# Kernel optimization log

Measured on AMD Instinct MI355X. Metric: run time of the kernel, lower is better.

The kernel has to match this reference:

```python
import jax, jax.numpy as jnp
import numpy as np

B, T, D = 8, 2048, 1024   # batch, seq_len (== block_size), n_embed
HS = 128                   # head_size

def setup_inputs() -> dict:
    key = jax.random.key(0)
    kx, kk, kq, kv = jax.random.split(key, 4)
    s = D ** -0.5  # torch Linear default init scale ~ U(-1/sqrt(in), 1/sqrt(in))
    x  = jax.random.normal(kx, (B, T, D), dtype=jnp.float32)
    Wk = jax.random.uniform(kk, (HS, D), jnp.float32, -s, s)
    Wq = jax.random.uniform(kq, (HS, D), jnp.float32, -s, s)
    Wv = jax.random.uniform(kv, (HS, D), jnp.float32, -s, s)
    return {"x": x, "Wk": Wk, "Wq": Wq, "Wv": Wv}

def reference(x, Wk, Wq, Wv):
    # single-head causal self-attention; dropout disabled (eval mode)
    Tlen = x.shape[1]
    k = jnp.einsum('btd,hd->bth', x, Wk)   # [B,T,HS]
    q = jnp.einsum('btd,hd->bth', x, Wq)
    v = jnp.einsum('btd,hd->bth', x, Wv)
    scale = Wk.shape[0] ** -0.5
    scores = jnp.einsum('bth,bsh->bts', q, k) * scale   # [B,T,T]
    causal = jnp.tril(jnp.ones((Tlen, Tlen), dtype=bool))
    scores = jnp.where(causal, scores, -jnp.inf)
    weights = jax.nn.softmax(scores, axis=-1)
    out = jnp.einsum('bts,bsh->bth', weights, v)        # [B,T,HS]
    return out
```

## Files before the change

kernel.cpp:

```cpp
#include <hip/hip_runtime.h>
#include <hip/hip_bf16.h>
#include <math.h>

#define BATCH_N 8
#define SEQ_T   2048
#define DIM_D   1024
#define HS_N    128

using bf16x8_t = __attribute__((ext_vector_type(8))) __bf16;
using bf16x4_t = __attribute__((ext_vector_type(4))) __bf16;
using f32x4_t  = __attribute__((ext_vector_type(4))) float;

__device__ __forceinline__ f32x4_t mfma_16x16x32(bf16x8_t a, bf16x8_t b, f32x4_t c) {
  return __builtin_amdgcn_mfma_f32_16x16x32_bf16(a, b, c, 0, 0, 0);
}

__device__ __forceinline__ void async_cp16(const void* g, void* l) {
  __builtin_amdgcn_global_load_lds(
      (const __attribute__((address_space(1))) unsigned int*)g,
      (__attribute__((address_space(3))) unsigned int*)l, 16, 0, 0);
}

#define BAR()      __builtin_amdgcn_s_barrier()
#define FENCE()    asm volatile("" ::: "memory")
#define WAIT_VM(n) asm volatile("s_waitcnt vmcnt(" #n ")" ::: "memory")
#define WAIT_LGKM0 asm volatile("s_waitcnt lgkmcnt(0)" ::: "memory")

__global__ __launch_bounds__(256) void castw_kernel(
    const float* __restrict__ Wk, const float* __restrict__ Wq,
    const float* __restrict__ Wv, __bf16* __restrict__ Wb,
    unsigned int* __restrict__ km) {
  if (blockIdx.x == 0 && threadIdx.x < 8) km[threadIdx.x] = 0u;
  int idx = blockIdx.x * 256 + threadIdx.x;
  int e   = idx * 4;
  int row = e >> 10;
  int col = e & 1023;
  const float* src;
  float sc = 1.0f;
  if (row < 128) {
    src = Wk + row * DIM_D + col;
  } else if (row < 256) {
    src = Wq + (row - 128) * DIM_D + col;
    sc  = 0.08838834764831845f;
  } else {
    src = Wv + (row - 256) * DIM_D + col;
  }
  float4 v = *(const float4*)src;
  bf16x4_t o;
  o[0] = (__bf16)(v.x * sc); o[1] = (__bf16)(v.y * sc);
  o[2] = (__bf16)(v.z * sc); o[3] = (__bf16)(v.w * sc);
  *(bf16x4_t*)(Wb + e) = o;
}

__global__ __launch_bounds__(512, 1) void proj_kernel(
    const float* __restrict__ x, const __bf16* __restrict__ Wb,
    __bf16* __restrict__ Qb, __bf16* __restrict__ Kb, __bf16* __restrict__ Vt,
    unsigned int* __restrict__ km) {
  __shared__ __align__(16) char psmem[139264];
  __bf16* A = (__bf16*)psmem;

  const int tid  = threadIdx.x;
  const int lane = tid & 63;
  const int wave = tid >> 6;
  const int h    = wave >> 2;
  const int g    = wave & 3;
  const int lr = lane & 15;
  const int lq = lane >> 4;
  const int m0 = blockIdx.x * 64;

  f32x4_t acc[2][6];
  #pragma unroll
  for (int mt = 0; mt < 2; ++mt)
    #pragma unroll
    for (int nt = 0; nt < 6; ++nt) acc[mt][nt] = (f32x4_t){0.f, 0.f, 0.f, 0.f};

  auto stageB = [&](int kt) {
    __bf16* Bs = (__bf16*)(psmem + 65536 + (kt % 3) * 24576);
    for (int c = wave; c < 24; c += 8) {
      const int row = c * 16 + (lane >> 2);
      const int u   = (lane & 3) ^ ((row >> 1) & 3);
      async_cp16(Wb + (size_t)row * DIM_D + kt * 32 + u * 8, Bs + c * 512);
    }
  };

  stageB(0);
  stageB(1);

  for (int p = 0; p < 2; ++p) {
    __syncthreads();

    {
      const int r  = tid >> 3;
      const int t  = tid & 7;
      const float* xs = x + (size_t)(m0 + r) * DIM_D + p * 512;
      __bf16* as = A + r * 512;
      const int sw = r & 7;
      #pragma unroll
      for (int i = 0; i < 8; ++i) {
        const int u = t + 8 * i;
        float4 f0 = *(const float4*)(xs + u * 8);
        float4 f1 = *(const float4*)(xs + u * 8 + 4);
        bf16x8_t a;
        a[0] = (__bf16)f0.x; a[1] = (__bf16)f0.y;
        a[2] = (__bf16)f0.z; a[3] = (__bf16)f0.w;
        a[4] = (__bf16)f1.x; a[5] = (__bf16)f1.y;
        a[6] = (__bf16)f1.z; a[7] = (__bf16)f1.w;
        *(bf16x8_t*)(as + ((u ^ sw) * 8)) = a;
      }
    }
    __syncthreads();

    for (int kt2 = 0; kt2 < 16; ++kt2) {
      const int kt = p * 16 + kt2;
      if (kt + 2 < 32) stageB(kt + 2);
      if (kt < 30)       { WAIT_VM(6); }
      else if (kt == 30) { WAIT_VM(3); }
      else               { WAIT_VM(0); }
      BAR();
      FENCE();
      const __bf16* Bs = (const __bf16*)(psmem + 65536 + (kt % 3) * 24576);

      bf16x8_t af[2];
      #pragma unroll
      for (int mt = 0; mt < 2; ++mt) {
        const int ml = h * 32 + mt * 16 + lr;
        const int u  = kt2 * 4 + lq;
        af[mt] = *(const bf16x8_t*)(&A[ml * 512 + ((u ^ (ml & 7)) * 8)]);
      }
      bf16x8_t bfv[6];
      #pragma unroll
      for (int nt = 0; nt < 6; ++nt) {
        const int nl = g * 96 + nt * 16 + lr;
        bfv[nt] = *(const bf16x8_t*)(&Bs[nl * 32 + ((lq ^ ((nl >> 1) & 3)) * 8)]);
      }
      #pragma unroll
      for (int mt = 0; mt < 2; ++mt)
        #pragma unroll
        for (int nt = 0; nt < 6; ++nt)
          acc[mt][nt] = mfma_16x16x32(af[mt], bfv[nt], acc[mt][nt]);
      WAIT_LGKM0;
      BAR();
      FENCE();
    }
  }

  __syncthreads();
  float* rowss = (float*)psmem;
  if (tid < 64) rowss[tid] = 0.f;
  __syncthreads();
  if (g < 2) {
    #pragma unroll
    for (int mt = 0; mt < 2; ++mt)
      #pragma unroll
      for (int r = 0; r < 4; ++r) {
        float s = 0.f;
        #pragma unroll
        for (int nt = 0; nt < 6; ++nt)
          if (g == 0 || nt < 2) s += acc[mt][nt][r] * acc[mt][nt][r];
        s += __shfl_xor(s, 1); s += __shfl_xor(s, 2);
        s += __shfl_xor(s, 4); s += __shfl_xor(s, 8);
        if (lr == 0) atomicAdd(&rowss[h * 32 + mt * 16 + lq * 4 + r], s);
      }
  }
  __syncthreads();
  if (tid < 64) {
    float v = rowss[tid];
    #pragma unroll
    for (int off = 1; off < 64; off <<= 1) v = fmaxf(v, __shfl_xor(v, off));
    if (tid == 0) atomicMax(km + (m0 >> 11), __float_as_uint(v));
  }

  #pragma unroll
  for (int mt = 0; mt < 2; ++mt) {
    const int t0 = m0 + h * 32 + mt * 16 + lq * 4;
    #pragma unroll
    for (int nt = 0; nt < 6; ++nt) {
      const int nn = g * 96 + nt * 16 + lr;
      if (nn < 256) {
        __bf16* dst = (nn < 128) ? (Kb + nn) : (Qb + (nn - 128));
        #pragma unroll
        for (int r = 0; r < 4; ++r)
          dst[(size_t)(t0 + r) * HS_N] = (__bf16)acc[mt][nt][r];
      } else {
        const int bb = t0 >> 11;
        const int tl = t0 & 2047;
        bf16x4_t o;
        #pragma unroll
        for (int r = 0; r < 4; ++r) o[r] = (__bf16)acc[mt][nt][r];
        *(bf16x4_t*)(Vt + (size_t)bb * (HS_N * SEQ_T) + (size_t)(nn - 256) * SEQ_T + tl) = o;
      }
    }
  }
}

__global__ __launch_bounds__(256, 2) void attn_kernel(
    const __bf16* __restrict__ Qb, const __bf16* __restrict__ Kb,
    const __bf16* __restrict__ Vt, const unsigned int* __restrict__ km,
    __bf16* __restrict__ Opart, float* __restrict__ lpart) {
  __shared__ __align__(16) char smem[81920];
  __bf16* KsBase = (__bf16*)smem;
  __bf16* VsBase = (__bf16*)(smem + 32768);
  float*  Ofl    = (float*)smem;

  const int lane = threadIdx.x & 63;
  const int wave = threadIdx.x >> 6;
  const int lr = lane & 15;
  const int lq = lane >> 4;
  const int bid  = blockIdx.x;
  const int b    = bid & 7;
  const int rest = bid >> 3;
  const int jg   = 15 - (rest >> 2);
  const int p4   = rest & 3;
  const int Q0   = jg * 128;
  const int qa   = Q0 + wave * 32;
  const int ch   = 2 * (jg + 1);
  const int c0   = (p4 * ch) >> 2;
  const int c1   = ((p4 + 1) * ch) >> 2;

  const __bf16* Qbb = Qb + (size_t)b * (SEQ_T * HS_N);
  const __bf16* Kbb = Kb + (size_t)b * (SEQ_T * HS_N);
  const __bf16* Vbb = Vt + (size_t)b * (HS_N * SEQ_T);
  __bf16* pbA = (__bf16*)(smem + 65536 + wave * 4096);
  __bf16* pbB = (__bf16*)(smem + 65536 + wave * 4096 + 2048);

  bf16x8_t qf[2][4];
  #pragma unroll
  for (int t = 0; t < 2; ++t)
    #pragma unroll
    for (int ks = 0; ks < 4; ++ks)
      qf[t][ks] = *(const bf16x8_t*)(Qbb + (size_t)(qa + t * 16 + lr) * HS_N
                                     + ks * 32 + lq * 8);

  const float km2 = __uint_as_float(km[b]);
  float mrow[2][4];
  #pragma unroll
  for (int t = 0; t < 2; ++t) {
    float qn2 = 0.f;
    #pragma unroll
    for (int ks = 0; ks < 4; ++ks)
      #pragma unroll
      for (int j = 0; j < 8; ++j) { float f = (float)qf[t][ks][j]; qn2 += f * f; }
    qn2 += __shfl_xor(qn2, 16);
    qn2 += __shfl_xor(qn2, 32);
    #pragma unroll
    for (int r2 = 0; r2 < 4; ++r2)
      mrow[t][r2] = sqrtf(__shfl(qn2, lq * 4 + r2) * km2);
  }

  f32x4_t Oa[2][8];
  #pragma unroll
  for (int t = 0; t < 2; ++t)
    #pragma unroll
    for (int o = 0; o < 8; ++o) Oa[t][o] = (f32x4_t){0.f, 0.f, 0.f, 0.f};
  float lsum[2][4] = {{0.f,0.f,0.f,0.f},{0.f,0.f,0.f,0.f}};

  auto stage = [&](int bufi, int c) {
    const int kk = c * 64;
    __bf16* Ks = KsBase + bufi * 8192;
    for (int idx = wave; idx < 32; idx += 4) {
      if (idx < 16) {
        const int row = idx * 4 + (lane >> 4);
        const int u   = (lane & 15) ^ (row & 15);
        async_cp16(Kbb + (size_t)(kk + row) * HS_N + u * 8, Ks + idx * 512);
      } else {
        const int i2  = idx - 16;
        const int row = i2 * 8 + (lane >> 3);
        const int u   = (lane & 7) ^ (row & 7);
        async_cp16(Vbb + (size_t)row * SEQ_T + kk + u * 8, VsBase + bufi * 8192 + i2 * 512);
      }
    }
  };

  if (c0 < c1) stage(0, c0);
  __syncthreads();

  for (int c = c0; c < c1; ++c) {
    const int cur = (c - c0) & 1;
    if (c + 1 < c1) {
      stage(cur ^ 1, c + 1);
      WAIT_VM(8);
    } else {
      WAIT_VM(0);
    }
    BAR();
    FENCE();

    const int kk = c * 64;
    const __bf16* Ks = KsBase + cur * 8192;
    const __bf16* Vs = VsBase + cur * 8192;

    f32x4_t s0[4], s1[4];
    #pragma unroll
    for (int nt = 0; nt < 4; ++nt) {
      s0[nt] = (f32x4_t){0.f, 0.f, 0.f, 0.f};
      s1[nt] = (f32x4_t){0.f, 0.f, 0.f, 0.f};
    }
    #pragma unroll
    for (int ks = 0; ks < 4; ++ks)
      #pragma unroll
      for (int nt = 0; nt < 4; ++nt) {
        bf16x8_t kf = *(const bf16x8_t*)(
            &Ks[(nt * 16 + lr) * 128 + (((ks * 4 + lq) ^ lr) * 8)]);
        s0[nt] = mfma_16x16x32(qf[0][ks], kf, s0[nt]);
        s1[nt] = mfma_16x16x32(qf[1][ks], kf, s1[nt]);
      }
    const int q0a = qa, q0b = qa + 16;
    if (kk + 63 > q0a) {
      #pragma unroll
      for (int nt = 0; nt < 4; ++nt) {
        const int col = kk + nt * 16 + lr;
        #pragma unroll
        for (int r2 = 0; r2 < 4; ++r2)
          if (col > q0a + lq * 4 + r2) s0[nt][r2] = -INFINITY;
      }
    }
    if (kk + 63 > q0b) {
      #pragma unroll
      for (int nt = 0; nt < 4; ++nt) {
        const int col = kk + nt * 16 + lr;
        #pragma unroll
        for (int r2 = 0; r2 < 4; ++r2)
          if (col > q0b + lq * 4 + r2) s1[nt][r2] = -INFINITY;
      }
    }

    #pragma unroll
    for (int r2 = 0; r2 < 4; ++r2) {
      float a0 = __expf(s0[0][r2] - mrow[0][r2]);
      float a1 = __expf(s0[1][r2] - mrow[0][r2]);
      float a2 = __expf(s0[2][r2] - mrow[0][r2]);
      float a3 = __expf(s0[3][r2] - mrow[0][r2]);
      s0[0][r2] = a0; s0[1][r2] = a1; s0[2][r2] = a2; s0[3][r2] = a3;
      lsum[0][r2] += (a0 + a1) + (a2 + a3);
      float b0 = __expf(s1[0][r2] - mrow[1][r2]);
      float b1 = __expf(s1[1][r2] - mrow[1][r2]);
      float b2 = __expf(s1[2][r2] - mrow[1][r2]);
      float b3 = __expf(s1[3][r2] - mrow[1][r2]);
      s1[0][r2] = b0; s1[1][r2] = b1; s1[2][r2] = b2; s1[3][r2] = b3;
      lsum[1][r2] += (b0 + b1) + (b2 + b3);
    }

    #pragma unroll
    for (int nt = 0; nt < 4; ++nt)
      #pragma unroll
      for (int r2 = 0; r2 < 4; ++r2) {
        const int prow = lq * 4 + r2;
        const int pcol = (nt * 16 + lr) ^ ((prow & 7) << 3);
        pbA[prow * 64 + pcol] = (__bf16)s0[nt][r2];
        pbB[prow * 64 + pcol] = (__bf16)s1[nt][r2];
      }

    #pragma unroll
    for (int k2 = 0; k2 < 2; ++k2) {
      const int au = ((k2 * 4 + lq) ^ (lr & 7)) << 3;
      bf16x8_t afrA = *(const bf16x8_t*)(pbA + lr * 64 + au);
      bf16x8_t afrB = *(const bf16x8_t*)(pbB + lr * 64 + au);
      #pragma unroll
      for (int o = 0; o < 8; ++o) {
        bf16x8_t vfr = *(const bf16x8_t*)(
            &Vs[(o * 16 + lr) * 64 + (((k2 * 4 + lq) ^ (lr & 7)) * 8)]);
        Oa[0][o] = mfma_16x16x32(afrA, vfr, Oa[0][o]);
        Oa[1][o] = mfma_16x16x32(afrB, vfr, Oa[1][o]);
      }
    }
    WAIT_LGKM0;
    BAR();
    FENCE();
  }

  #pragma unroll
  for (int t = 0; t < 2; ++t)
    #pragma unroll
    for (int r2 = 0; r2 < 4; ++r2) {
      float v = lsum[t][r2];
      v += __shfl_xor(v, 1);
      v += __shfl_xor(v, 2);
      v += __shfl_xor(v, 4);
      v += __shfl_xor(v, 8);
      if (lr == 0)
        lpart[bid * 128 + wave * 32 + t * 16 + lq * 4 + r2] = v;
    }

  #pragma unroll
  for (int t = 0; t < 2; ++t)
    #pragma unroll
    for (int o = 0; o < 8; ++o)
      #pragma unroll
      for (int r2 = 0; r2 < 4; ++r2)
        Ofl[(wave * 32 + t * 16 + lq * 4 + r2) * 132 + o * 16 + lr] = Oa[t][o][r2];
  __syncthreads();

  {
    const int row = threadIdx.x >> 1;
    const int cb  = (threadIdx.x & 1) * 64;
    __bf16* dst = Opart + ((size_t)bid * 128 + row) * 128 + cb;
    #pragma unroll
    for (int g2 = 0; g2 < 16; ++g2) {
      float4 f = *(const float4*)(&Ofl[row * 132 + cb + g2 * 4]);
      bf16x4_t o;
      o[0] = (__bf16)f.x; o[1] = (__bf16)f.y; o[2] = (__bf16)f.z; o[3] = (__bf16)f.w;
      *(bf16x4_t*)(dst + g2 * 4) = o;
    }
  }
}

__global__ __launch_bounds__(256) void merge_kernel(
    const __bf16* __restrict__ Opart, const float* __restrict__ lpart,
    float* __restrict__ out) {
  const int idx = blockIdx.x * 256 + threadIdx.x;
  const int row = idx >> 5;
  const int c4  = (idx & 31) * 4;
  const int b   = row >> 11;
  const int tl  = row & 2047;
  const int jg  = tl >> 7;
  const int lrow = tl & 127;
  const int rbase = (15 - jg) * 4;
  float a0 = 0.f, a1 = 0.f, a2 = 0.f, a3 = 0.f, l = 0.f;
  #pragma unroll
  for (int p = 0; p < 4; ++p) {
    const int s = b + 8 * (rbase + p);
    bf16x4_t a = *(const bf16x4_t*)(Opart + ((size_t)s * 128 + lrow) * 128 + c4);
    a0 += (float)a[0]; a1 += (float)a[1]; a2 += (float)a[2]; a3 += (float)a[3];
    l += lpart[s * 128 + lrow];
  }
  const float inv = 1.0f / l;
  float4 o;
  o.x = a0 * inv; o.y = a1 * inv; o.z = a2 * inv; o.w = a3 * inv;
  *(float4*)(out + (size_t)row * HS_N + c4) = o;
}

extern "C" void kernel_launch(void* const* d_in, const int* in_sizes, int n_in,
                              void* d_out, int out_size, void* d_ws, size_t ws_size,
                              hipStream_t stream) {
  const float* x  = (const float*)d_in[0];
  const float* Wk = (const float*)d_in[1];
  const float* Wq = (const float*)d_in[2];
  const float* Wv = (const float*)d_in[3];
  float* out = (float*)d_out;

  char* ws = (char*)d_ws;
  __bf16* Wb = (__bf16*)ws;
  __bf16* Qb = (__bf16*)(ws + 786432);
  __bf16* Kb = (__bf16*)(ws + 786432 + 4194304);
  __bf16* Vt = (__bf16*)(ws + 786432 + 8388608);
  unsigned int* km = (unsigned int*)(ws + 13369344);
  __bf16* Opart = (__bf16*)(ws + 13369600);
  float*  lpart = (float*)(ws + 30146816);

  castw_kernel<<<384, 256, 0, stream>>>(Wk, Wq, Wv, Wb, km);
  proj_kernel<<<256, 512, 0, stream>>>(x, Wb, Qb, Kb, Vt, km);
  attn_kernel<<<512, 256, 0, stream>>>(Qb, Kb, Vt, km, Opart, lpart);
  merge_kernel<<<2048, 256, 0, stream>>>(Opart, lpart, out);
}
```

Baseline: 151.3 us.

## Stream x tiles asynchronously into LDS and halve projection block size

The projection kernel now uses 32-row blocks of 256 threads, aiming for two blocks per CU, instead of 64-row blocks of 512 threads. The x tile is no longer converted to bf16 by every thread in two bulk phases. It is fetched as fp32 by async global-to-LDS copies, double-buffered alongside the weight tiles, and converted to bf16 just before the MFMA. This overlaps x loading with compute and removes the bulk-conversion stalls and extra barriers. In exchange, each block re-reads the full weight matrix for fewer rows, doubling weight traffic, and the fp32-to-bf16 conversion now happens on every k-step.

```diff
diff --git a/kernel.cpp b/kernel.cpp
--- a/kernel.cpp
+++ b/kernel.cpp
@@ -52,21 +52,18 @@
   *(bf16x4_t*)(Wb + e) = o;
 }
 
-__global__ __launch_bounds__(512, 1) void proj_kernel(
+__global__ __launch_bounds__(256, 2) void proj_kernel(
     const float* __restrict__ x, const __bf16* __restrict__ Wb,
     __bf16* __restrict__ Qb, __bf16* __restrict__ Kb, __bf16* __restrict__ Vt,
     unsigned int* __restrict__ km) {
-  __shared__ __align__(16) char psmem[139264];
-  __bf16* A = (__bf16*)psmem;
+  __shared__ __align__(16) char psmem[57344];
 
   const int tid  = threadIdx.x;
   const int lane = tid & 63;
   const int wave = tid >> 6;
-  const int h    = wave >> 2;
-  const int g    = wave & 3;
   const int lr = lane & 15;
   const int lq = lane >> 4;
-  const int m0 = blockIdx.x * 64;
+  const int m0 = blockIdx.x * 32;
 
   f32x4_t acc[2][6];
   #pragma unroll
@@ -74,81 +71,77 @@
     #pragma unroll
     for (int nt = 0; nt < 6; ++nt) acc[mt][nt] = (f32x4_t){0.f, 0.f, 0.f, 0.f};
 
+  auto stageA = [&](int kt) {
+    char* As = psmem + (kt & 1) * 4096;
+    const int row = wave * 8 + (lane >> 3);
+    const int u16 = lane & 7;
+    const int su16 = (((u16 >> 1) ^ (row & 3)) << 1) | (u16 & 1);
+    async_cp16(x + (size_t)(m0 + row) * DIM_D + kt * 32 + su16 * 4,
+               As + wave * 1024);
+  };
+
   auto stageB = [&](int kt) {
-    __bf16* Bs = (__bf16*)(psmem + 65536 + (kt % 3) * 24576);
-    for (int c = wave; c < 24; c += 8) {
+    __bf16* Bs = (__bf16*)(psmem + 8192 + (kt & 1) * 24576);
+    for (int c = wave; c < 24; c += 4) {
       const int row = c * 16 + (lane >> 2);
       const int u   = (lane & 3) ^ ((row >> 1) & 3);
       async_cp16(Wb + (size_t)row * DIM_D + kt * 32 + u * 8, Bs + c * 512);
     }
   };
 
+  stageA(0);
   stageB(0);
-  stageB(1);
-
-  for (int p = 0; p < 2; ++p) {
-    __syncthreads();
-
-    {
-      const int r  = tid >> 3;
-      const int t  = tid & 7;
-      const float* xs = x + (size_t)(m0 + r) * DIM_D + p * 512;
-      __bf16* as = A + r * 512;
-      const int sw = r & 7;
-      #pragma unroll
-      for (int i = 0; i < 8; ++i) {
-        const int u = t + 8 * i;
-        float4 f0 = *(const float4*)(xs + u * 8);
-        float4 f1 = *(const float4*)(xs + u * 8 + 4);
-        bf16x8_t a;
-        a[0] = (__bf16)f0.x; a[1] = (__bf16)f0.y;
-        a[2] = (__bf16)f0.z; a[3] = (__bf16)f0.w;
-        a[4] = (__bf16)f1.x; a[5] = (__bf16)f1.y;
-        a[6] = (__bf16)f1.z; a[7] = (__bf16)f1.w;
-        *(bf16x8_t*)(as + ((u ^ sw) * 8)) = a;
-      }
-    }
-    __syncthreads();
-
-    for (int kt2 = 0; kt2 < 16; ++kt2) {
-      const int kt = p * 16 + kt2;
-      if (kt + 2 < 32) stageB(kt + 2);
-      if (kt < 30)       { WAIT_VM(6); }
-      else if (kt == 30) { WAIT_VM(3); }
-      else               { WAIT_VM(0); }
-      BAR();
-      FENCE();
-      const __bf16* Bs = (const __bf16*)(psmem + 65536 + (kt % 3) * 24576);
-
-      bf16x8_t af[2];
-      #pragma unroll
-      for (int mt = 0; mt < 2; ++mt) {
-        const int ml = h * 32 + mt * 16 + lr;
-        const int u  = kt2 * 4 + lq;
-        af[mt] = *(const bf16x8_t*)(&A[ml * 512 + ((u ^ (ml & 7)) * 8)]);
-      }
-      bf16x8_t bfv[6];
-      #pragma unroll
-      for (int nt = 0; nt < 6; ++nt) {
-        const int nl = g * 96 + nt * 16 + lr;
-        bfv[nt] = *(const bf16x8_t*)(&Bs[nl * 32 + ((lq ^ ((nl >> 1) & 3)) * 8)]);
-      }
-      #pragma unroll
-      for (int mt = 0; mt < 2; ++mt)
-        #pragma unroll
-        for (int nt = 0; nt < 6; ++nt)
-          acc[mt][nt] = mfma_16x16x32(af[mt], bfv[nt], acc[mt][nt]);
-      WAIT_LGKM0;
-      BAR();
-      FENCE();
-    }
+  __syncthreads();
+
+  for (int kt = 0; kt < 32; ++kt) {
+    if (kt + 1 < 32) {
+      stageA(kt + 1);
+      stageB(kt + 1);
+      WAIT_VM(7);
+    } else {
+      WAIT_VM(0);
+    }
+    BAR();
+    FENCE();
+
+    const float*  As = (const float*)(psmem + (kt & 1) * 4096);
+    const __bf16* Bs = (const __bf16*)(psmem + 8192 + (kt & 1) * 24576);
+
+    bf16x8_t af[2];
+    #pragma unroll
+    for (int mt = 0; mt < 2; ++mt) {
+      const int ml   = mt * 16 + lr;
+      const int u32r = lq ^ (ml & 3);
+      f32x4_t lo = *(const f32x4_t*)(As + ml * 32 + u32r * 8);
+      f32x4_t hi = *(const f32x4_t*)(As + ml * 32 + u32r * 8 + 4);
+      bf16x8_t a;
+      a[0] = (__bf16)lo[0]; a[1] = (__bf16)lo[1];
+      a[2] = (__bf16)lo[2]; a[3] = (__bf16)lo[3];
+      a[4] = (__bf16)hi[0]; a[5] = (__bf16)hi[1];
+      a[6] = (__bf16)hi[2]; a[7] = (__bf16)hi[3];
+      af[mt] = a;
+    }
+    bf16x8_t bfv[6];
+    #pragma unroll
+    for (int nt = 0; nt < 6; ++nt) {
+      const int nl = wave * 96 + nt * 16 + lr;
+      bfv[nt] = *(const bf16x8_t*)(&Bs[nl * 32 + ((lq ^ ((nl >> 1) & 3)) * 8)]);
+    }
+    #pragma unroll
+    for (int mt = 0; mt < 2; ++mt)
+      #pragma unroll
+      for (int nt = 0; nt < 6; ++nt)
+        acc[mt][nt] = mfma_16x16x32(af[mt], bfv[nt], acc[mt][nt]);
+    WAIT_LGKM0;
+    BAR();
+    FENCE();
   }
 
   __syncthreads();
   float* rowss = (float*)psmem;
-  if (tid < 64) rowss[tid] = 0.f;
-  __syncthreads();
-  if (g < 2) {
+  if (tid < 32) rowss[tid] = 0.f;
+  __syncthreads();
+  if (wave < 2) {
     #pragma unroll
     for (int mt = 0; mt < 2; ++mt)
       #pragma unroll
@@ -156,26 +149,26 @@
         float s = 0.f;
         #pragma unroll
         for (int nt = 0; nt < 6; ++nt)
-          if (g == 0 || nt < 2) s += acc[mt][nt][r] * acc[mt][nt][r];
+          if (wave == 0 || nt < 2) s += acc[mt][nt][r] * acc[mt][nt][r];
         s += __shfl_xor(s, 1); s += __shfl_xor(s, 2);
         s += __shfl_xor(s, 4); s += __shfl_xor(s, 8);
-        if (lr == 0) atomicAdd(&rowss[h * 32 + mt * 16 + lq * 4 + r], s);
-      }
-  }
-  __syncthreads();
-  if (tid < 64) {
+        if (lr == 0) atomicAdd(&rowss[mt * 16 + lq * 4 + r], s);
+      }
+  }
+  __syncthreads();
+  if (tid < 32) {
     float v = rowss[tid];
     #pragma unroll
-    for (int off = 1; off < 64; off <<= 1) v = fmaxf(v, __shfl_xor(v, off));
+    for (int off = 1; off < 32; off <<= 1) v = fmaxf(v, __shfl_xor(v, off));
     if (tid == 0) atomicMax(km + (m0 >> 11), __float_as_uint(v));
   }
 
   #pragma unroll
   for (int mt = 0; mt < 2; ++mt) {
-    const int t0 = m0 + h * 32 + mt * 16 + lq * 4;
+    const int t0 = m0 + mt * 16 + lq * 4;
     #pragma unroll
     for (int nt = 0; nt < 6; ++nt) {
-      const int nn = g * 96 + nt * 16 + lr;
+      const int nn = wave * 96 + nt * 16 + lr;
       if (nn < 256) {
         __bf16* dst = (nn < 128) ? (Kb + nn) : (Qb + (nn - 128));
         #pragma unroll
@@ -448,7 +441,7 @@
   float*  lpart = (float*)(ws + 30146816);
 
   castw_kernel<<<384, 256, 0, stream>>>(Wk, Wq, Wv, Wb, km);
-  proj_kernel<<<256, 512, 0, stream>>>(x, Wb, Qb, Kb, Vt, km);
+  proj_kernel<<<512, 256, 0, stream>>>(x, Wb, Qb, Kb, Vt, km);
   attn_kernel<<<512, 256, 0, stream>>>(Qb, Kb, Vt, km, Opart, lpart);
   merge_kernel<<<2048, 256, 0, stream>>>(Opart, lpart, out);
 }
```

Result: slower. 165.0 us (+9.0%).

## Split projection into 32-row blocks with per-wave private weight buffers, dropping barriers

Applied to the files above, without the earlier changes.

The projection kernel now runs 512 blocks of 256 threads over 32 rows each, instead of 256 blocks of 512 threads over 64 rows. Each wave stages only its own 96 weight rows into a private double buffer, so the two block-wide barriers in every k-step go away and only per-wave waits remain. This also shrinks shared memory so two blocks can share a CU. The trade-off is that every block reloads the full weight matrix for half as many rows, which doubles weight traffic, and the pipeline is shallower (two stages instead of three).

```diff
diff --git a/kernel.cpp b/kernel.cpp
--- a/kernel.cpp
+++ b/kernel.cpp
@@ -52,21 +52,19 @@
   *(bf16x4_t*)(Wb + e) = o;
 }
 
-__global__ __launch_bounds__(512, 1) void proj_kernel(
+__global__ __launch_bounds__(256, 2) void proj_kernel(
     const float* __restrict__ x, const __bf16* __restrict__ Wb,
     __bf16* __restrict__ Qb, __bf16* __restrict__ Kb, __bf16* __restrict__ Vt,
     unsigned int* __restrict__ km) {
-  __shared__ __align__(16) char psmem[139264];
+  __shared__ __align__(16) char psmem[81920];
   __bf16* A = (__bf16*)psmem;
 
   const int tid  = threadIdx.x;
   const int lane = tid & 63;
   const int wave = tid >> 6;
-  const int h    = wave >> 2;
-  const int g    = wave & 3;
   const int lr = lane & 15;
   const int lq = lane >> 4;
-  const int m0 = blockIdx.x * 64;
+  const int m0 = blockIdx.x * 32;
 
   f32x4_t acc[2][6];
   #pragma unroll
@@ -74,17 +72,20 @@
     #pragma unroll
     for (int nt = 0; nt < 6; ++nt) acc[mt][nt] = (f32x4_t){0.f, 0.f, 0.f, 0.f};
 
+  __bf16* BsBase = (__bf16*)(psmem + 32768 + wave * 12288);
+
   auto stageB = [&](int kt) {
-    __bf16* Bs = (__bf16*)(psmem + 65536 + (kt % 3) * 24576);
-    for (int c = wave; c < 24; c += 8) {
-      const int row = c * 16 + (lane >> 2);
-      const int u   = (lane & 3) ^ ((row >> 1) & 3);
+    __bf16* Bs = BsBase + (kt & 1) * 3072;
+    #pragma unroll
+    for (int c = 0; c < 6; ++c) {
+      const int rl  = c * 16 + (lane >> 2);
+      const int row = wave * 96 + rl;
+      const int u   = (lane & 3) ^ ((rl >> 1) & 3);
       async_cp16(Wb + (size_t)row * DIM_D + kt * 32 + u * 8, Bs + c * 512);
     }
   };
 
   stageB(0);
-  stageB(1);
 
   for (int p = 0; p < 2; ++p) {
     __syncthreads();
@@ -112,26 +113,28 @@
 
     for (int kt2 = 0; kt2 < 16; ++kt2) {
       const int kt = p * 16 + kt2;
-      if (kt + 2 < 32) stageB(kt + 2);
-      if (kt < 30)       { WAIT_VM(6); }
-      else if (kt == 30) { WAIT_VM(3); }
-      else               { WAIT_VM(0); }
-      BAR();
+      if (kt + 1 < 32) {
+        stageB(kt + 1);
+        WAIT_VM(6);
+      } else {
+        WAIT_VM(0);
+      }
       FENCE();
-      const __bf16* Bs = (const __bf16*)(psmem + 65536 + (kt % 3) * 24576);
+
+      const __bf16* Bs = BsBase + (kt & 1) * 3072;
 
       bf16x8_t af[2];
       #pragma unroll
       for (int mt = 0; mt < 2; ++mt) {
-        const int ml = h * 32 + mt * 16 + lr;
+        const int ml = mt * 16 + lr;
         const int u  = kt2 * 4 + lq;
         af[mt] = *(const bf16x8_t*)(&A[ml * 512 + ((u ^ (ml & 7)) * 8)]);
       }
       bf16x8_t bfv[6];
       #pragma unroll
       for (int nt = 0; nt < 6; ++nt) {
-        const int nl = g * 96 + nt * 16 + lr;
-        bfv[nt] = *(const bf16x8_t*)(&Bs[nl * 32 + ((lq ^ ((nl >> 1) & 3)) * 8)]);
+        const int rl = nt * 16 + lr;
+        bfv[nt] = *(const bf16x8_t*)(&Bs[rl * 32 + ((lq ^ ((rl >> 1) & 3)) * 8)]);
       }
       #pragma unroll
       for (int mt = 0; mt < 2; ++mt)
@@ -139,16 +142,15 @@
         for (int nt = 0; nt < 6; ++nt)
           acc[mt][nt] = mfma_16x16x32(af[mt], bfv[nt], acc[mt][nt]);
       WAIT_LGKM0;
-      BAR();
       FENCE();
     }
   }
 
   __syncthreads();
   float* rowss = (float*)psmem;
-  if (tid < 64) rowss[tid] = 0.f;
+  if (tid < 32) rowss[tid] = 0.f;
   __syncthreads();
-  if (g < 2) {
+  if (wave < 2) {
     #pragma unroll
     for (int mt = 0; mt < 2; ++mt)
       #pragma unroll
@@ -156,26 +158,26 @@
         float s = 0.f;
         #pragma unroll
         for (int nt = 0; nt < 6; ++nt)
-          if (g == 0 || nt < 2) s += acc[mt][nt][r] * acc[mt][nt][r];
+          if (wave == 0 || nt < 2) s += acc[mt][nt][r] * acc[mt][nt][r];
         s += __shfl_xor(s, 1); s += __shfl_xor(s, 2);
         s += __shfl_xor(s, 4); s += __shfl_xor(s, 8);
-        if (lr == 0) atomicAdd(&rowss[h * 32 + mt * 16 + lq * 4 + r], s);
+        if (lr == 0) atomicAdd(&rowss[mt * 16 + lq * 4 + r], s);
       }
   }
   __syncthreads();
-  if (tid < 64) {
+  if (tid < 32) {
     float v = rowss[tid];
     #pragma unroll
-    for (int off = 1; off < 64; off <<= 1) v = fmaxf(v, __shfl_xor(v, off));
+    for (int off = 1; off < 32; off <<= 1) v = fmaxf(v, __shfl_xor(v, off));
     if (tid == 0) atomicMax(km + (m0 >> 11), __float_as_uint(v));
   }
 
   #pragma unroll
   for (int mt = 0; mt < 2; ++mt) {
-    const int t0 = m0 + h * 32 + mt * 16 + lq * 4;
+    const int t0 = m0 + mt * 16 + lq * 4;
     #pragma unroll
     for (int nt = 0; nt < 6; ++nt) {
-      const int nn = g * 96 + nt * 16 + lr;
+      const int nn = wave * 96 + nt * 16 + lr;
       if (nn < 256) {
         __bf16* dst = (nn < 128) ? (Kb + nn) : (Qb + (nn - 128));
         #pragma unroll
@@ -448,7 +450,7 @@
   float*  lpart = (float*)(ws + 30146816);
 
   castw_kernel<<<384, 256, 0, stream>>>(Wk, Wq, Wv, Wb, km);
-  proj_kernel<<<256, 512, 0, stream>>>(x, Wb, Qb, Kb, Vt, km);
+  proj_kernel<<<512, 256, 0, stream>>>(x, Wb, Qb, Kb, Vt, km);
   attn_kernel<<<512, 256, 0, stream>>>(Qb, Kb, Vt, km, Opart, lpart);
   merge_kernel<<<2048, 256, 0, stream>>>(Opart, lpart, out);
 }
```

After: 157.3 us. 1.04x slower.
